# Performance work log

Measured on AMD Instinct MI355X. Metric: run time of the kernel, lower is better.

Reference implementation:

```python
import jax, jax.numpy as jnp
import numpy as np

DIM = 2048
N_HEADS = 16
Q_LORA = 1536
KV_LORA = 512
NOPE = 128
ROPE = 64
V_DIM = 128
QK_HEAD = NOPE + ROPE
SEQ = 4096
THETA = 10000.0
EPS = 1e-6
SCALE = QK_HEAD ** -0.5  # max_seq_len==4096 not >4096, so no mscale adjustment


def rms_norm(x, w):
    return x * jax.lax.rsqrt(jnp.mean(x * x, axis=-1, keepdims=True) + EPS) * w


def rope_cos_sin(seqlen):
    inv_freq = 1.0 / THETA ** (jnp.arange(0, ROPE, 2, dtype=jnp.float32) / ROPE)  # [ROPE/2]
    t = jnp.arange(seqlen, dtype=jnp.float32)
    freqs = jnp.outer(t, inv_freq)  # [S, ROPE/2]
    return jnp.cos(freqs), jnp.sin(freqs)


def apply_rope(x, cos, sin):
    # x: (b, s, h, ROPE); pairs (x0, x1) rotated as complex mult, interleaved layout
    b, s, h, d = x.shape
    xr = x.reshape(b, s, h, d // 2, 2)
    x0, x1 = xr[..., 0], xr[..., 1]
    c = cos[None, :, None, :]
    sn = sin[None, :, None, :]
    out = jnp.stack([x0 * c - x1 * sn, x0 * sn + x1 * c], axis=-1)
    return out.reshape(b, s, h, d)


def setup_inputs() -> dict:
    key = jax.random.key(0)
    ks = jax.random.split(key, 8)
    s = lambda fan_in: 1.0 / np.sqrt(fan_in)
    return {
        "x": jax.random.normal(ks[0], (1, SEQ, DIM), jnp.float32),
        "wq_a_w": jax.random.normal(ks[1], (Q_LORA, DIM), jnp.float32) * s(DIM),
        "q_norm_w": 1.0 + 0.02 * jax.random.normal(ks[2], (Q_LORA,), jnp.float32),
        "wq_b_w": jax.random.normal(ks[3], (N_HEADS * QK_HEAD, Q_LORA), jnp.float32) * s(Q_LORA),
        "wkv_a_w": jax.random.normal(ks[4], (KV_LORA + ROPE, DIM), jnp.float32) * s(DIM),
        "kv_norm_w": 1.0 + 0.02 * jax.random.normal(ks[5], (KV_LORA,), jnp.float32),
        "wkv_b_w": jax.random.normal(ks[6], (N_HEADS * (NOPE + V_DIM), KV_LORA), jnp.float32) * s(KV_LORA),
        "wo_w": jax.random.normal(ks[7], (DIM, DIM), jnp.float32) * s(DIM),
    }


def reference(x, wq_a_w, q_norm_w, wq_b_w, wkv_a_w, kv_norm_w, wkv_b_w, wo_w):
    b, seqlen, _ = x.shape
    cos, sin = rope_cos_sin(seqlen)

    # Q path: low-rank down-proj -> RMSNorm -> up-proj
    q = rms_norm(x @ wq_a_w.T, q_norm_w) @ wq_b_w.T
    q = q.reshape(b, seqlen, N_HEADS, QK_HEAD)
    q_nope, q_pe = q[..., :NOPE], q[..., NOPE:]
    q_pe = apply_rope(q_pe, cos, sin)

    # KV path: compressed latent + decoupled rope key
    kv_a = x @ wkv_a_w.T  # (b, s, KV_LORA + ROPE)
    kv_latent, k_pe_raw = kv_a[..., :KV_LORA], kv_a[..., KV_LORA:]
    kv = rms_norm(kv_latent, kv_norm_w)               # (b, t, c)
    k_pe = apply_rope(k_pe_raw[:, :, None, :], cos, sin)[:, :, 0, :]  # (b, t, r)

    # Absorption trick: fold wkv_b's K-part into q_nope, attend against latents
    wkv_b = wkv_b_w.reshape(N_HEADS, NOPE + V_DIM, KV_LORA)
    q_abs = jnp.einsum("bshd,hdc->bshc", q_nope, wkv_b[:, :NOPE])

    scores = (jnp.einsum("bshc,btc->bsht", q_abs, kv)
              + jnp.einsum("bshr,btr->bsht", q_pe, k_pe)) * SCALE

    # causal additive mask over (s_query, t_key)
    causal = jnp.tril(jnp.ones((seqlen, seqlen), dtype=bool))
    scores = jnp.where(causal[None, :, None, :], scores, jnp.float32(-1e30))
    attn = jax.nn.softmax(scores, axis=-1)

    # post-softmax: aggregate latents, then recover V via wkv_b's V-part
    ctx = jnp.einsum("bsht,btc->bshc", attn, kv)
    v = jnp.einsum("bshc,hdc->bshd", ctx, wkv_b[:, NOPE:])  # (b, s, h, V_DIM)
    out = v.reshape(b, seqlen, N_HEADS * V_DIM) @ wo_w.T
    return out
```

## Files before the change

kernel.cpp:

```cpp
#include <hip/hip_runtime.h>

typedef unsigned short u16;
typedef __attribute__((ext_vector_type(8))) short bf16x8;
typedef __attribute__((ext_vector_type(4))) float f32x4;
typedef __attribute__((ext_vector_type(4))) unsigned short u16x4;

#define MFMA16(a, b, c) __builtin_amdgcn_mfma_f32_16x16x32_bf16((a), (b), (c), 0, 0, 0)

#define SEQ 4096
#define SCALE 0.07216878364870323f
#define LOGTHETA 9.210340371976184f

__device__ __forceinline__ u16 f2bf(float f) {
  union { float f; unsigned u; } c; c.f = f;
  unsigned u = c.u;
  unsigned r = (u + 0x7fffu + ((u >> 16) & 1u)) >> 16;
  return (u16)r;
}
__device__ __forceinline__ float bf2f(u16 b) {
  union { unsigned u; float f; } c; c.u = ((unsigned)b) << 16;
  return c.f;
}

__global__ void cvt_bf16(const float* __restrict__ src, u16* __restrict__ dst, int n4) {
  int stride = gridDim.x * blockDim.x;
  for (int i = blockIdx.x * blockDim.x + threadIdx.x; i < n4; i += stride) {
    f32x4 v = ((const f32x4*)src)[i];
    u16x4 o;
    o[0] = f2bf(v[0]); o[1] = f2bf(v[1]); o[2] = f2bf(v[2]); o[3] = f2bf(v[3]);
    ((u16x4*)dst)[i] = o;
  }
}

__global__ void trans_wkvb(const u16* __restrict__ w, u16* __restrict__ wt) {
  int stride = gridDim.x * blockDim.x;
  for (int i = blockIdx.x * blockDim.x + threadIdx.x; i < 16 * 512 * 128; i += stride) {
    int h = i >> 16;
    int r = i & 65535;
    int c = r >> 7, d = r & 127;
    wt[i] = w[(h * 256 + d) * 512 + c];
  }
}

__global__ void trans_vt(const u16* __restrict__ kva, u16* __restrict__ vt2) {
  __shared__ u16 tile[64][65];
  int c0 = blockIdx.x * 64;
  int t0 = blockIdx.y * 64;
  for (int k = 0; k < 16; k++) {
    int el = threadIdx.x + k * 256;
    int r = el >> 6, c = el & 63;
    tile[r][c] = kva[(t0 + r) * 576 + c0 + c];
  }
  __syncthreads();
  for (int k = 0; k < 16; k++) {
    int el = threadIdx.x + k * 256;
    int r = el >> 6, c = el & 63;
    int t = t0 + c;
    vt2[(t >> 5) * 16384 + (c0 + r) * 32 + (t & 31)] = tile[c][r];
  }
}

__global__ void rms_q_kernel(u16* __restrict__ qa, const float* __restrict__ w) {
  int row = blockIdx.x;
  u16* p = qa + row * 1536;
  float vals[6];
  float ss = 0.f;
#pragma unroll
  for (int k = 0; k < 6; k++) {
    float v = bf2f(p[threadIdx.x + k * 256]);
    vals[k] = v;
    ss += v * v;
  }
  for (int m = 1; m < 64; m <<= 1) ss += __shfl_xor(ss, m);
  __shared__ float red[4];
  int wid = threadIdx.x >> 6;
  if ((threadIdx.x & 63) == 0) red[wid] = ss;
  __syncthreads();
  float tot = red[0] + red[1] + red[2] + red[3];
  float rr = rsqrtf(tot / 1536.f + 1e-6f);
#pragma unroll
  for (int k = 0; k < 6; k++) {
    int i = threadIdx.x + k * 256;
    p[i] = f2bf(vals[k] * rr * w[i]);
  }
}

__global__ void rms_kv_kernel(u16* __restrict__ kva, const float* __restrict__ w) {
  int t = blockIdx.x;
  u16* p = kva + t * 576;
  float v0 = bf2f(p[threadIdx.x]);
  float v1 = bf2f(p[threadIdx.x + 256]);
  float ss = v0 * v0 + v1 * v1;
  for (int m = 1; m < 64; m <<= 1) ss += __shfl_xor(ss, m);
  __shared__ float red[4];
  int wid = threadIdx.x >> 6;
  if ((threadIdx.x & 63) == 0) red[wid] = ss;
  __syncthreads();
  float tot = red[0] + red[1] + red[2] + red[3];
  float rr = rsqrtf(tot / 512.f + 1e-6f);
  p[threadIdx.x] = f2bf(v0 * rr * w[threadIdx.x]);
  p[threadIdx.x + 256] = f2bf(v1 * rr * w[threadIdx.x + 256]);
  if (threadIdx.x < 32) {
    int i = threadIdx.x;
    float x0 = bf2f(p[512 + 2 * i]);
    float x1 = bf2f(p[512 + 2 * i + 1]);
    float invf = expf(-((float)(2 * i) / 64.f) * LOGTHETA);
    float ang = (float)t * invf;
    float cs = cosf(ang), sn = sinf(ang);
    p[512 + 2 * i] = f2bf(x0 * cs - x1 * sn);
    p[512 + 2 * i + 1] = f2bf(x0 * sn + x1 * cs);
  }
}

__global__ void rope_q_kernel(const u16* __restrict__ qb, u16* __restrict__ qcat) {
  int stride = gridDim.x * blockDim.x;
  for (int idx = blockIdx.x * blockDim.x + threadIdx.x; idx < 4096 * 512; idx += stride) {
    int s = idx >> 9;
    int r = idx & 511;
    int h = r >> 5, i = r & 31;
    float x0 = bf2f(qb[s * 3072 + h * 192 + 128 + 2 * i]);
    float x1 = bf2f(qb[s * 3072 + h * 192 + 128 + 2 * i + 1]);
    float invf = expf(-((float)(2 * i) / 64.f) * LOGTHETA);
    float ang = (float)s * invf;
    float cs = cosf(ang) * SCALE, sn = sinf(ang) * SCALE;
    qcat[s * 9216 + h * 576 + 512 + 2 * i] = f2bf(x0 * cs - x1 * sn);
    qcat[s * 9216 + h * 576 + 512 + 2 * i + 1] = f2bf(x0 * sn + x1 * cs);
  }
}

template <int BN, bool OUTF32>
__launch_bounds__(256)
__global__ void gemm_tiled(const u16* __restrict__ A, int lda, int az,
                           const u16* __restrict__ W, int ldw, int wz,
                           void* __restrict__ Cp, int ldc, int cz, int K, float oscale) {
  constexpr int NCH = 8 + BN / 16;
  constexpr int NBF = BN / 32;
  __shared__ __align__(16) u16 lds[2][NCH * 512];

  int z = blockIdx.z;
  int wid = threadIdx.x >> 6, lane = threadIdx.x & 63;
  int quad = lane >> 4, l16 = lane & 15;
  int wr = wid >> 1, wc = wid & 1;
  int m0 = blockIdx.y * 128;
  int n0 = blockIdx.x * BN;

  const u16* Az = A + (size_t)z * az;
  const u16* Wz = W + (size_t)z * wz;

  f32x4 acc[4][NBF];
#pragma unroll
  for (int i = 0; i < 4; i++)
#pragma unroll
    for (int j = 0; j < NBF; j++) acc[i][j] = {0.f, 0.f, 0.f, 0.f};

#pragma unroll
  for (int jj = 0; jj < NCH / 4; jj++) {
    int c = jj * 4 + wid;
    const u16* src = (c < 8) ? (Az + (m0 + c * 16 + l16) * (size_t)lda + quad * 8)
                             : (Wz + (n0 + (c - 8) * 16 + l16) * (size_t)ldw + quad * 8);
    __builtin_amdgcn_global_load_lds(
        (const __attribute__((address_space(1))) unsigned int*)src,
        (__attribute__((address_space(3))) unsigned int*)&lds[0][c * 512], 16, 0, 0);
  }

  int buf = 0;
  for (int k0 = 0; k0 < K; k0 += 32) {
    __syncthreads();
    if (k0 + 32 < K) {
      int k1 = k0 + 32;
#pragma unroll
      for (int jj = 0; jj < NCH / 4; jj++) {
        int c = jj * 4 + wid;
        const u16* src = (c < 8) ? (Az + (m0 + c * 16 + l16) * (size_t)lda + k1 + quad * 8)
                                 : (Wz + (n0 + (c - 8) * 16 + l16) * (size_t)ldw + k1 + quad * 8);
        __builtin_amdgcn_global_load_lds(
            (const __attribute__((address_space(1))) unsigned int*)src,
            (__attribute__((address_space(3))) unsigned int*)&lds[buf ^ 1][c * 512], 16, 0, 0);
      }
    }
    const u16* base = &lds[buf][0];
    bf16x8 a[4], b[NBF];
#pragma unroll
    for (int i = 0; i < 4; i++)
      a[i] = *(const bf16x8*)(base + (wr * 4 + i) * 512 + lane * 8);
#pragma unroll
    for (int j = 0; j < NBF; j++)
      b[j] = *(const bf16x8*)(base + (8 + wc * NBF + j) * 512 + lane * 8);
#pragma unroll
    for (int i = 0; i < 4; i++)
#pragma unroll
      for (int j = 0; j < NBF; j++) acc[i][j] = MFMA16(a[i], b[j], acc[i][j]);
    buf ^= 1;
  }

#pragma unroll
  for (int i = 0; i < 4; i++) {
    int row = m0 + wr * 64 + i * 16 + quad * 4;
#pragma unroll
    for (int j = 0; j < NBF; j++) {
      int col = n0 + wc * (BN / 2) + j * 16 + l16;
#pragma unroll
      for (int r = 0; r < 4; r++) {
        size_t cbase = (size_t)z * cz + (size_t)(row + r) * ldc + col;
        if (OUTF32) ((float*)Cp)[cbase] = acc[i][j][r] * oscale;
        else        ((u16*)Cp)[cbase] = f2bf(acc[i][j][r] * oscale);
      }
    }
  }
}

__launch_bounds__(512, 2)
__global__ void attn_kernel(const u16* __restrict__ qcat, const u16* __restrict__ kcat,
                            const u16* __restrict__ vt2, u16* __restrict__ ctx) {
  __shared__ __align__(16) u16 lds[2][34816];
  __shared__ __align__(16) u16 plds[8][16][40];

  int wid = threadIdx.x >> 6, lane = threadIdx.x & 63;
  int quad = lane >> 4, l16 = lane & 15;
  int bx = blockIdx.x;
  int h = bx & 15;
  int jb = 31 - (bx >> 4);
  int qb0 = jb << 7;
  int m0 = qb0 + wid * 16;

  bf16x8 q[18];
  {
    const u16* qb = qcat + (m0 + l16) * 9216 + h * 576 + quad * 8;
#pragma unroll
    for (int kk = 0; kk < 18; kk++) q[kk] = *(const bf16x8*)(qb + kk * 32);
  }

  f32x4 zero = {0.f, 0.f, 0.f, 0.f};
  f32x4 o[32];
#pragma unroll
  for (int ct = 0; ct < 32; ct++) o[ct] = zero;
  float li[4] = {0.f, 0.f, 0.f, 0.f};

  int nt = (qb0 >> 5) + 4;

  const u16* sp[9];
  int sstr[9], soff[9];
  bool sact[9];
#pragma unroll
  for (int jj = 0; jj < 9; jj++) {
    int c = jj * 8 + wid;
    sact[jj] = (c < 68);
    soff[jj] = c * 512;
    if (c < 36) {
      int kk = c >> 1, half = c & 1;
      sp[jj] = kcat + (half * 16 + l16) * 576 + kk * 32 + quad * 8;
      sstr[jj] = 32 * 576;
    } else {
      int ct = c - 36;
      sp[jj] = vt2 + (ct * 16 + l16) * 32 + quad * 8;
      sstr[jj] = 16384;
    }
  }

#pragma unroll
  for (int jj = 0; jj < 9; jj++) {
    if (sact[jj]) {
      __builtin_amdgcn_global_load_lds(
          (const __attribute__((address_space(1))) unsigned int*)sp[jj],
          (__attribute__((address_space(3))) unsigned int*)&lds[0][soff[jj]], 16, 0, 0);
      sp[jj] += sstr[jj];
    }
  }

  for (int ti = 0; ti < nt; ti++) {
    __syncthreads();
    int buf = ti & 1;
    if (ti + 1 < nt) {
      u16* dbase = &lds[buf ^ 1][0];
#pragma unroll
      for (int jj = 0; jj < 9; jj++) {
        if (sact[jj]) {
          __builtin_amdgcn_global_load_lds(
              (const __attribute__((address_space(1))) unsigned int*)sp[jj],
              (__attribute__((address_space(3))) unsigned int*)&dbase[soff[jj]], 16, 0, 0);
          sp[jj] += sstr[jj];
        }
      }
    }

    int t0 = ti << 5;
    if (t0 <= m0 + 15) {
      const u16* kb = &lds[buf][0];
      const u16* vb = &lds[buf][18432];
      f32x4 s0 = zero, s1 = zero;
#pragma unroll
      for (int kk = 0; kk < 18; kk++) {
        bf16x8 b0 = *(const bf16x8*)(&kb[(kk * 2 + 0) * 512 + lane * 8]);
        bf16x8 b1 = *(const bf16x8*)(&kb[(kk * 2 + 1) * 512 + lane * 8]);
        s0 = MFMA16(q[kk], b0, s0);
        s1 = MFMA16(q[kk], b1, s1);
      }
      int tc0 = t0 + l16, tc1 = t0 + 16 + l16;
#pragma unroll
      for (int r = 0; r < 4; r++) {
        int mrow = m0 + quad * 4 + r;
        float e0 = (tc0 <= mrow) ? __expf(s0[r]) : 0.f;
        float e1 = (tc1 <= mrow) ? __expf(s1[r]) : 0.f;
        li[r] += e0 + e1;
        plds[wid][quad * 4 + r][l16] = f2bf(e0);
        plds[wid][quad * 4 + r][16 + l16] = f2bf(e1);
      }
      __threadfence_block();
      bf16x8 ap = *(const bf16x8*)(&plds[wid][l16][quad * 8]);
#pragma unroll
      for (int ct = 0; ct < 32; ct++) {
        bf16x8 bv = *(const bf16x8*)(&vb[ct * 512 + lane * 8]);
        o[ct] = MFMA16(ap, bv, o[ct]);
      }
    }
  }

#pragma unroll
  for (int r = 0; r < 4; r++) {
    float s = li[r];
    s += __shfl_xor(s, 1);
    s += __shfl_xor(s, 2);
    s += __shfl_xor(s, 4);
    s += __shfl_xor(s, 8);
    li[r] = s;
  }
  f32x4 inv = {1.f / li[0], 1.f / li[1], 1.f / li[2], 1.f / li[3]};
#pragma unroll
  for (int ct = 0; ct < 32; ct++) {
    f32x4 val = o[ct] * inv;
    int base = (m0 + quad * 4) * 8192 + h * 512 + ct * 16 + l16;
    ctx[base] = f2bf(val[0]);
    ctx[base + 8192] = f2bf(val[1]);
    ctx[base + 2 * 8192] = f2bf(val[2]);
    ctx[base + 3 * 8192] = f2bf(val[3]);
  }
}

extern "C" void kernel_launch(void* const* d_in, const int* in_sizes, int n_in,
                              void* d_out, int out_size, void* d_ws, size_t ws_size,
                              hipStream_t stream) {
  const float* x = (const float*)d_in[0];
  const float* wqa = (const float*)d_in[1];
  const float* qnw = (const float*)d_in[2];
  const float* wqb = (const float*)d_in[3];
  const float* wkva = (const float*)d_in[4];
  const float* kvnw = (const float*)d_in[5];
  const float* wkvb = (const float*)d_in[6];
  const float* wo = (const float*)d_in[7];

  u16* ws = (u16*)d_ws;
  u16* XB = ws;
  u16* WQAB = ws + 8388608;
  u16* WQBB = ws + 11534336;
  u16* WKVAB = ws + 16252928;
  u16* WKVBB = ws + 17432576;
  u16* WKVBT = ws + 19529728;
  u16* WOB = ws + 20578304;
  u16* QA = ws + 24772608;
  u16* KVA = ws + 31064064;
  u16* VT = ws + 33423360;
  u16* QCAT = ws + 35520512;
  u16* CTX = ws + 73269248;
  u16* QB = CTX;
  u16* VBUF = QCAT;

  dim3 blk(256);

  cvt_bf16<<<1024, blk, 0, stream>>>(x, XB, 2097152);
  cvt_bf16<<<1024, blk, 0, stream>>>(wqa, WQAB, 786432);
  cvt_bf16<<<1024, blk, 0, stream>>>(wqb, WQBB, 1179648);
  cvt_bf16<<<1024, blk, 0, stream>>>(wkva, WKVAB, 294912);
  cvt_bf16<<<1024, blk, 0, stream>>>(wkvb, WKVBB, 524288);
  cvt_bf16<<<1024, blk, 0, stream>>>(wo, WOB, 1048576);
  trans_wkvb<<<1024, blk, 0, stream>>>(WKVBB, WKVBT);

  gemm_tiled<128, false><<<dim3(12, 32, 1), blk, 0, stream>>>(XB, 2048, 0, WQAB, 2048, 0, QA, 1536, 0, 2048, 1.f);
  gemm_tiled<64, false><<<dim3(9, 32, 1), blk, 0, stream>>>(XB, 2048, 0, WKVAB, 2048, 0, KVA, 576, 0, 2048, 1.f);

  rms_q_kernel<<<4096, blk, 0, stream>>>(QA, qnw);
  rms_kv_kernel<<<4096, blk, 0, stream>>>(KVA, kvnw);
  trans_vt<<<dim3(8, 64), blk, 0, stream>>>(KVA, VT);

  gemm_tiled<128, false><<<dim3(24, 32, 1), blk, 0, stream>>>(QA, 1536, 0, WQBB, 1536, 0, QB, 3072, 0, 1536, 1.f);

  gemm_tiled<128, false><<<dim3(4, 32, 16), blk, 0, stream>>>(QB, 3072, 192, WKVBT, 128, 65536, QCAT, 9216, 576, 128, SCALE);
  rope_q_kernel<<<2048, blk, 0, stream>>>(QB, QCAT);

  attn_kernel<<<512, dim3(512), 0, stream>>>(QCAT, KVA, VT, CTX);

  gemm_tiled<128, false><<<dim3(1, 32, 16), blk, 0, stream>>>(CTX, 8192, 512, WKVBB + 65536, 512, 131072, VBUF, 2048, 128, 512, 1.f);

  gemm_tiled<128, true><<<dim3(16, 32, 1), blk, 0, stream>>>(VBUF, 2048, 0, WOB, 2048, 0, d_out, 2048, 0, 2048, 1.f);
}
```

Measured before the change: 928.2 us.

## Split PV stage by output columns across waves with shared P tile

In the attention kernel, the P·V stage now has each wave own 64 latent columns for all 128 query rows, instead of all 512 columns for its own 16 rows. Probabilities go through a block-wide shared-memory tile behind an extra barrier. Each wave therefore loads only 4 V fragments per tile and keeps them in registers, rather than reading all 32 V fragments from LDS. The QK loop uses two accumulator chains and s_setprio around the MFMA sections, and the final normalisation reads per-row inverse sums from LDS. The cost is one extra __syncthreads per key tile and coupling between waves that have different causal extents.

```diff
diff --git a/kernel.cpp b/kernel.cpp
--- a/kernel.cpp
+++ b/kernel.cpp
@@ -213,7 +213,8 @@
 __global__ void attn_kernel(const u16* __restrict__ qcat, const u16* __restrict__ kcat,
                             const u16* __restrict__ vt2, u16* __restrict__ ctx) {
   __shared__ __align__(16) u16 lds[2][34816];
-  __shared__ __align__(16) u16 plds[8][16][40];
+  __shared__ __align__(16) u16 plds[128][40];
+  __shared__ __align__(16) float linv[128];
 
   int wid = threadIdx.x >> 6, lane = threadIdx.x & 63;
   int quad = lane >> 4, l16 = lane & 15;
@@ -222,6 +223,7 @@
   int jb = 31 - (bx >> 4);
   int qb0 = jb << 7;
   int m0 = qb0 + wid * 16;
+  int cw0 = wid << 6;
 
   bf16x8 q[18];
   {
@@ -231,9 +233,11 @@
   }
 
   f32x4 zero = {0.f, 0.f, 0.f, 0.f};
-  f32x4 o[32];
-#pragma unroll
-  for (int ct = 0; ct < 32; ct++) o[ct] = zero;
+  f32x4 o[8][4];
+#pragma unroll
+  for (int rt = 0; rt < 8; rt++)
+#pragma unroll
+    for (int ct = 0; ct < 4; ct++) o[rt][ct] = zero;
   float li[4] = {0.f, 0.f, 0.f, 0.f};
 
   int nt = (qb0 >> 5) + 4;
@@ -286,15 +290,22 @@
     int t0 = ti << 5;
     if (t0 <= m0 + 15) {
       const u16* kb = &lds[buf][0];
-      const u16* vb = &lds[buf][18432];
-      f32x4 s0 = zero, s1 = zero;
-#pragma unroll
-      for (int kk = 0; kk < 18; kk++) {
-        bf16x8 b0 = *(const bf16x8*)(&kb[(kk * 2 + 0) * 512 + lane * 8]);
-        bf16x8 b1 = *(const bf16x8*)(&kb[(kk * 2 + 1) * 512 + lane * 8]);
-        s0 = MFMA16(q[kk], b0, s0);
-        s1 = MFMA16(q[kk], b1, s1);
-      }
+      f32x4 s0a = zero, s0b = zero, s1a = zero, s1b = zero;
+      __builtin_amdgcn_s_setprio(1);
+#pragma unroll
+      for (int kk = 0; kk < 18; kk += 2) {
+        bf16x8 b00 = *(const bf16x8*)(&kb[(kk * 2 + 0) * 512 + lane * 8]);
+        bf16x8 b01 = *(const bf16x8*)(&kb[(kk * 2 + 1) * 512 + lane * 8]);
+        bf16x8 b10 = *(const bf16x8*)(&kb[(kk * 2 + 2) * 512 + lane * 8]);
+        bf16x8 b11 = *(const bf16x8*)(&kb[(kk * 2 + 3) * 512 + lane * 8]);
+        s0a = MFMA16(q[kk], b00, s0a);
+        s1a = MFMA16(q[kk], b01, s1a);
+        s0b = MFMA16(q[kk + 1], b10, s0b);
+        s1b = MFMA16(q[kk + 1], b11, s1b);
+      }
+      __builtin_amdgcn_s_setprio(0);
+      f32x4 s0 = s0a + s0b;
+      f32x4 s1 = s1a + s1b;
       int tc0 = t0 + l16, tc1 = t0 + 16 + l16;
 #pragma unroll
       for (int r = 0; r < 4; r++) {
@@ -302,16 +313,31 @@
         float e0 = (tc0 <= mrow) ? __expf(s0[r]) : 0.f;
         float e1 = (tc1 <= mrow) ? __expf(s1[r]) : 0.f;
         li[r] += e0 + e1;
-        plds[wid][quad * 4 + r][l16] = f2bf(e0);
-        plds[wid][quad * 4 + r][16 + l16] = f2bf(e1);
-      }
-      __threadfence_block();
-      bf16x8 ap = *(const bf16x8*)(&plds[wid][l16][quad * 8]);
-#pragma unroll
-      for (int ct = 0; ct < 32; ct++) {
-        bf16x8 bv = *(const bf16x8*)(&vb[ct * 512 + lane * 8]);
-        o[ct] = MFMA16(ap, bv, o[ct]);
-      }
+        int rb = (wid << 4) + quad * 4 + r;
+        plds[rb][l16] = f2bf(e0);
+        plds[rb][16 + l16] = f2bf(e1);
+      }
+    }
+    __syncthreads();
+
+    {
+      const u16* vb = &lds[buf][18432];
+      bf16x8 bv0 = *(const bf16x8*)(&vb[(cw0 / 16 + 0) * 512 + lane * 8]);
+      bf16x8 bv1 = *(const bf16x8*)(&vb[(cw0 / 16 + 1) * 512 + lane * 8]);
+      bf16x8 bv2 = *(const bf16x8*)(&vb[(cw0 / 16 + 2) * 512 + lane * 8]);
+      bf16x8 bv3 = *(const bf16x8*)(&vb[(cw0 / 16 + 3) * 512 + lane * 8]);
+      __builtin_amdgcn_s_setprio(1);
+#pragma unroll
+      for (int rt = 0; rt < 8; rt++) {
+        if (t0 <= qb0 + rt * 16 + 15) {
+          bf16x8 ap = *(const bf16x8*)(&plds[rt * 16 + l16][quad * 8]);
+          o[rt][0] = MFMA16(ap, bv0, o[rt][0]);
+          o[rt][1] = MFMA16(ap, bv1, o[rt][1]);
+          o[rt][2] = MFMA16(ap, bv2, o[rt][2]);
+          o[rt][3] = MFMA16(ap, bv3, o[rt][3]);
+        }
+      }
+      __builtin_amdgcn_s_setprio(0);
     }
   }
 
@@ -324,15 +350,23 @@
     s += __shfl_xor(s, 8);
     li[r] = s;
   }
-  f32x4 inv = {1.f / li[0], 1.f / li[1], 1.f / li[2], 1.f / li[3]};
-#pragma unroll
-  for (int ct = 0; ct < 32; ct++) {
-    f32x4 val = o[ct] * inv;
-    int base = (m0 + quad * 4) * 8192 + h * 512 + ct * 16 + l16;
-    ctx[base] = f2bf(val[0]);
-    ctx[base + 8192] = f2bf(val[1]);
-    ctx[base + 2 * 8192] = f2bf(val[2]);
-    ctx[base + 3 * 8192] = f2bf(val[3]);
+  if (l16 == 0) {
+#pragma unroll
+    for (int r = 0; r < 4; r++) linv[(wid << 4) + quad * 4 + r] = 1.f / li[r];
+  }
+  __syncthreads();
+#pragma unroll
+  for (int rt = 0; rt < 8; rt++) {
+    f32x4 iv = *(const f32x4*)(&linv[rt * 16 + quad * 4]);
+#pragma unroll
+    for (int ct = 0; ct < 4; ct++) {
+      f32x4 val = o[rt][ct];
+      int base = (qb0 + rt * 16 + quad * 4) * 8192 + h * 512 + cw0 + ct * 16 + l16;
+      ctx[base] = f2bf(val[0] * iv[0]);
+      ctx[base + 8192] = f2bf(val[1] * iv[1]);
+      ctx[base + 2 * 8192] = f2bf(val[2] * iv[2]);
+      ctx[base + 3 * 8192] = f2bf(val[3] * iv[3]);
+    }
   }
 }
 
```

New measurement: 1.015 ms. 9.3% more time.

## Compute QK scores with 32x32 MFMA split across wave pairs

Applied to the files above, without the earlier changes.

The score computation moves from two 16x16x32 MFMAs per k-step in each wave to a 32x32x16 MFMA. Each pair of waves shares a 32-row query group, and each wave covers half of the 576-wide reduction dimension. The partial scores are exchanged through LDS and summed, which halves per-wave QK MFMA work and the K fragment reads. In exchange it adds an LDS exchange plus a block-wide barrier on every tile, a shared-memory path for the row sums, and extra synchronisation that could stall waves whose causal work has already ended.

```diff
diff --git a/kernel.cpp b/kernel.cpp
--- a/kernel.cpp
+++ b/kernel.cpp
@@ -3,9 +3,11 @@
 typedef unsigned short u16;
 typedef __attribute__((ext_vector_type(8))) short bf16x8;
 typedef __attribute__((ext_vector_type(4))) float f32x4;
+typedef __attribute__((ext_vector_type(16))) float f32x16;
 typedef __attribute__((ext_vector_type(4))) unsigned short u16x4;
 
 #define MFMA16(a, b, c) __builtin_amdgcn_mfma_f32_16x16x32_bf16((a), (b), (c), 0, 0, 0)
+#define MFMA32(a, b, c) __builtin_amdgcn_mfma_f32_32x32x16_bf16((a), (b), (c), 0, 0, 0)
 
 #define SEQ 4096
 #define SCALE 0.07216878364870323f
@@ -213,28 +215,32 @@
 __global__ void attn_kernel(const u16* __restrict__ qcat, const u16* __restrict__ kcat,
                             const u16* __restrict__ vt2, u16* __restrict__ ctx) {
   __shared__ __align__(16) u16 lds[2][34816];
-  __shared__ __align__(16) u16 plds[8][16][40];
+  __shared__ __align__(16) float exch[4][32][32];
+  __shared__ __align__(16) float linv[128];
 
   int wid = threadIdx.x >> 6, lane = threadIdx.x & 63;
   int quad = lane >> 4, l16 = lane & 15;
+  int l32 = lane & 31, hi = lane >> 5;
+  int pg = wid >> 1, ws = wid & 1;
   int bx = blockIdx.x;
   int h = bx & 15;
   int jb = 31 - (bx >> 4);
   int qb0 = jb << 7;
   int m0 = qb0 + wid * 16;
+  int pgm0 = qb0 + pg * 32;
 
   bf16x8 q[18];
   {
-    const u16* qb = qcat + (m0 + l16) * 9216 + h * 576 + quad * 8;
-#pragma unroll
-    for (int kk = 0; kk < 18; kk++) q[kk] = *(const bf16x8*)(qb + kk * 32);
+    const u16* qb = qcat + (size_t)(pgm0 + l32) * 9216 + h * 576 + ws * 288 + hi * 8;
+#pragma unroll
+    for (int kk = 0; kk < 18; kk++) q[kk] = *(const bf16x8*)(qb + kk * 16);
   }
 
   f32x4 zero = {0.f, 0.f, 0.f, 0.f};
   f32x4 o[32];
 #pragma unroll
   for (int ct = 0; ct < 32; ct++) o[ct] = zero;
-  float li[4] = {0.f, 0.f, 0.f, 0.f};
+  float li[8] = {0.f, 0.f, 0.f, 0.f, 0.f, 0.f, 0.f, 0.f};
 
   int nt = (qb0 >> 5) + 4;
 
@@ -247,8 +253,7 @@
     sact[jj] = (c < 68);
     soff[jj] = c * 512;
     if (c < 36) {
-      int kk = c >> 1, half = c & 1;
-      sp[jj] = kcat + (half * 16 + l16) * 576 + kk * 32 + quad * 8;
+      sp[jj] = kcat + (size_t)l32 * 576 + c * 16 + hi * 8;
       sstr[jj] = 32 * 576;
     } else {
       int ct = c - 36;
@@ -284,29 +289,66 @@
     }
 
     int t0 = ti << 5;
-    if (t0 <= m0 + 15) {
+    bool pact = (t0 <= pgm0 + 31);
+    f32x16 s;
+    if (pact) {
       const u16* kb = &lds[buf][0];
+      s = (f32x16){0.f, 0.f, 0.f, 0.f, 0.f, 0.f, 0.f, 0.f,
+                   0.f, 0.f, 0.f, 0.f, 0.f, 0.f, 0.f, 0.f};
+#pragma unroll
+      for (int kk = 0; kk < 18; kk++) {
+        bf16x8 kf = *(const bf16x8*)(&kb[(ws * 18 + kk) * 512 + lane * 8]);
+        s = MFMA32(q[kk], kf, s);
+      }
+      if (ws == 0) {
+#pragma unroll
+        for (int r8 = 0; r8 < 8; r8++) {
+          int rowl = (r8 & 3) + 8 * (r8 >> 2) + 4 * hi;
+          exch[pg][16 + rowl][l32] = s[r8 + 8];
+        }
+      } else {
+#pragma unroll
+        for (int r8 = 0; r8 < 8; r8++) {
+          int rowl = (r8 & 3) + 8 * (r8 >> 2) + 4 * hi;
+          exch[pg][rowl][l32] = s[r8];
+        }
+      }
+    }
+    asm volatile("s_waitcnt lgkmcnt(0)" ::: "memory");
+    __builtin_amdgcn_s_barrier();
+    __builtin_amdgcn_sched_barrier(0);
+
+    if (pact) {
       const u16* vb = &lds[buf][18432];
-      f32x4 s0 = zero, s1 = zero;
-#pragma unroll
-      for (int kk = 0; kk < 18; kk++) {
-        bf16x8 b0 = *(const bf16x8*)(&kb[(kk * 2 + 0) * 512 + lane * 8]);
-        bf16x8 b1 = *(const bf16x8*)(&kb[(kk * 2 + 1) * 512 + lane * 8]);
-        s0 = MFMA16(q[kk], b0, s0);
-        s1 = MFMA16(q[kk], b1, s1);
-      }
-      int tc0 = t0 + l16, tc1 = t0 + 16 + l16;
-#pragma unroll
-      for (int r = 0; r < 4; r++) {
-        int mrow = m0 + quad * 4 + r;
-        float e0 = (tc0 <= mrow) ? __expf(s0[r]) : 0.f;
-        float e1 = (tc1 <= mrow) ? __expf(s1[r]) : 0.f;
-        li[r] += e0 + e1;
-        plds[wid][quad * 4 + r][l16] = f2bf(e0);
-        plds[wid][quad * 4 + r][16 + l16] = f2bf(e1);
+      u16* Pu = (u16*)&exch[pg][ws * 16][0];
+      int tc = t0 + l32;
+      float ev[8];
+      if (ws == 0) {
+#pragma unroll
+        for (int r8 = 0; r8 < 8; r8++) {
+          int rowl = (r8 & 3) + 8 * (r8 >> 2) + 4 * hi;
+          float v = s[r8] + exch[pg][rowl][l32];
+          float e = (tc <= pgm0 + rowl) ? __expf(v) : 0.f;
+          li[r8] += e;
+          ev[r8] = e;
+        }
+      } else {
+#pragma unroll
+        for (int r8 = 0; r8 < 8; r8++) {
+          int rowl = (r8 & 3) + 8 * (r8 >> 2) + 4 * hi;
+          float v = s[r8 + 8] + exch[pg][16 + rowl][l32];
+          float e = (tc <= pgm0 + 16 + rowl) ? __expf(v) : 0.f;
+          li[r8] += e;
+          ev[r8] = e;
+        }
+      }
+#pragma unroll
+      for (int r8 = 0; r8 < 8; r8++) {
+        int rowl = (r8 & 3) + 8 * (r8 >> 2) + 4 * hi;
+        Pu[rowl * 40 + l32] = f2bf(ev[r8]);
       }
       __threadfence_block();
-      bf16x8 ap = *(const bf16x8*)(&plds[wid][l16][quad * 8]);
+      bf16x8 ap = *(const bf16x8*)(&Pu[l16 * 40 + quad * 8]);
 #pragma unroll
       for (int ct = 0; ct < 32; ct++) {
         bf16x8 bv = *(const bf16x8*)(&vb[ct * 512 + lane * 8]);
@@ -316,23 +358,32 @@
   }
 
 #pragma unroll
-  for (int r = 0; r < 4; r++) {
-    float s = li[r];
-    s += __shfl_xor(s, 1);
-    s += __shfl_xor(s, 2);
-    s += __shfl_xor(s, 4);
-    s += __shfl_xor(s, 8);
-    li[r] = s;
-  }
-  f32x4 inv = {1.f / li[0], 1.f / li[1], 1.f / li[2], 1.f / li[3]};
+  for (int r8 = 0; r8 < 8; r8++) {
+    float sum = li[r8];
+    sum += __shfl_xor(sum, 1);
+    sum += __shfl_xor(sum, 2);
+    sum += __shfl_xor(sum, 4);
+    sum += __shfl_xor(sum, 8);
+    sum += __shfl_xor(sum, 16);
+    li[r8] = sum;
+  }
+  if (l32 == 0) {
+#pragma unroll
+    for (int r8 = 0; r8 < 8; r8++) {
+      int rowl = (r8 & 3) + 8 * (r8 >> 2) + 4 * hi;
+      linv[wid * 16 + rowl] = 1.f / li[r8];
+    }
+  }
+  __syncthreads();
+  f32x4 iv = *(const f32x4*)(&linv[wid * 16 + quad * 4]);
 #pragma unroll
   for (int ct = 0; ct < 32; ct++) {
-    f32x4 val = o[ct] * inv;
+    f32x4 val = o[ct];
     int base = (m0 + quad * 4) * 8192 + h * 512 + ct * 16 + l16;
-    ctx[base] = f2bf(val[0]);
-    ctx[base + 8192] = f2bf(val[1]);
-    ctx[base + 2 * 8192] = f2bf(val[2]);
-    ctx[base + 3 * 8192] = f2bf(val[3]);
+    ctx[base] = f2bf(val[0] * iv[0]);
+    ctx[base + 8192] = f2bf(val[1] * iv[1]);
+    ctx[base + 2 * 8192] = f2bf(val[2] * iv[2]);
+    ctx[base + 3 * 8192] = f2bf(val[3] * iv[3]);
   }
 }
 
```

Result: slower. 1.214 ms (+30.8%).

## Split attention LDS into single K and V buffers with staggered prefetch

Applied to the files above, without the earlier changes.

Replaces the double-buffered combined K/V LDS tile with single K and V buffers. V for the current tile is loaded at the start of each iteration, and the next K tile is loaded after the QK MFMAs finish, behind an explicit waitcnt and barrier. This roughly halves LDS use, which may allow more blocks per CU, but it exposes V-load latency before the PV MFMAs. It also remaps block indices so heads are interleaved across query blocks for better L2 locality, and adds setprio around the MFMA loops.

```diff
diff --git a/kernel.cpp b/kernel.cpp
--- a/kernel.cpp
+++ b/kernel.cpp
@@ -212,14 +212,16 @@
 __launch_bounds__(512, 2)
 __global__ void attn_kernel(const u16* __restrict__ qcat, const u16* __restrict__ kcat,
                             const u16* __restrict__ vt2, u16* __restrict__ ctx) {
-  __shared__ __align__(16) u16 lds[2][34816];
+  __shared__ __align__(16) u16 kbuf[18432];
+  __shared__ __align__(16) u16 vbuf[16384];
   __shared__ __align__(16) u16 plds[8][16][40];
+  __shared__ __align__(16) float linv[128];
 
   int wid = threadIdx.x >> 6, lane = threadIdx.x & 63;
   int quad = lane >> 4, l16 = lane & 15;
   int bx = blockIdx.x;
-  int h = bx & 15;
-  int jb = 31 - (bx >> 4);
+  int h = (bx >> 3) & 15;
+  int jb = 31 - (((bx >> 7) << 3) | (bx & 7));
   int qb0 = jb << 7;
   int m0 = qb0 + wid * 16;
 
@@ -238,63 +240,76 @@
 
   int nt = (qb0 >> 5) + 4;
 
-  const u16* sp[9];
-  int sstr[9], soff[9];
-  bool sact[9];
-#pragma unroll
-  for (int jj = 0; jj < 9; jj++) {
+  const u16* kp[5]; int koff[5]; bool kact[5];
+#pragma unroll
+  for (int jj = 0; jj < 5; jj++) {
     int c = jj * 8 + wid;
-    sact[jj] = (c < 68);
-    soff[jj] = c * 512;
-    if (c < 36) {
-      int kk = c >> 1, half = c & 1;
-      sp[jj] = kcat + (half * 16 + l16) * 576 + kk * 32 + quad * 8;
-      sstr[jj] = 32 * 576;
-    } else {
-      int ct = c - 36;
-      sp[jj] = vt2 + (ct * 16 + l16) * 32 + quad * 8;
-      sstr[jj] = 16384;
-    }
-  }
-
-#pragma unroll
-  for (int jj = 0; jj < 9; jj++) {
-    if (sact[jj]) {
+    kact[jj] = (c < 36);
+    koff[jj] = c * 512;
+    int kk = c >> 1, half = c & 1;
+    kp[jj] = kcat + (half * 16 + l16) * 576 + kk * 32 + quad * 8;
+  }
+  const u16* vp[4]; int voff[4];
+#pragma unroll
+  for (int jj = 0; jj < 4; jj++) {
+    int c = jj * 8 + wid;
+    voff[jj] = c * 512;
+    vp[jj] = vt2 + (c * 16 + l16) * 32 + quad * 8;
+  }
+
+#pragma unroll
+  for (int jj = 0; jj < 5; jj++) {
+    if (kact[jj]) {
       __builtin_amdgcn_global_load_lds(
-          (const __attribute__((address_space(1))) unsigned int*)sp[jj],
-          (__attribute__((address_space(3))) unsigned int*)&lds[0][soff[jj]], 16, 0, 0);
-      sp[jj] += sstr[jj];
+          (const __attribute__((address_space(1))) unsigned int*)kp[jj],
+          (__attribute__((address_space(3))) unsigned int*)&kbuf[koff[jj]], 16, 0, 0);
+      kp[jj] += 32 * 576;
     }
   }
 
   for (int ti = 0; ti < nt; ti++) {
     __syncthreads();
-    int buf = ti & 1;
-    if (ti + 1 < nt) {
-      u16* dbase = &lds[buf ^ 1][0];
-#pragma unroll
-      for (int jj = 0; jj < 9; jj++) {
-        if (sact[jj]) {
-          __builtin_amdgcn_global_load_lds(
-              (const __attribute__((address_space(1))) unsigned int*)sp[jj],
-              (__attribute__((address_space(3))) unsigned int*)&dbase[soff[jj]], 16, 0, 0);
-          sp[jj] += sstr[jj];
-        }
-      }
+
+#pragma unroll
+    for (int jj = 0; jj < 4; jj++) {
+      __builtin_amdgcn_global_load_lds(
+          (const __attribute__((address_space(1))) unsigned int*)vp[jj],
+          (__attribute__((address_space(3))) unsigned int*)&vbuf[voff[jj]], 16, 0, 0);
+      vp[jj] += 16384;
     }
 
     int t0 = ti << 5;
-    if (t0 <= m0 + 15) {
-      const u16* kb = &lds[buf][0];
-      const u16* vb = &lds[buf][18432];
-      f32x4 s0 = zero, s1 = zero;
+    bool act = (t0 <= m0 + 15);
+    f32x4 s0 = zero, s1 = zero;
+    if (act) {
+      __builtin_amdgcn_s_setprio(1);
 #pragma unroll
       for (int kk = 0; kk < 18; kk++) {
-        bf16x8 b0 = *(const bf16x8*)(&kb[(kk * 2 + 0) * 512 + lane * 8]);
-        bf16x8 b1 = *(const bf16x8*)(&kb[(kk * 2 + 1) * 512 + lane * 8]);
+        bf16x8 b0 = *(const bf16x8*)(&kbuf[(kk * 2 + 0) * 512 + lane * 8]);
+        bf16x8 b1 = *(const bf16x8*)(&kbuf[(kk * 2 + 1) * 512 + lane * 8]);
         s0 = MFMA16(q[kk], b0, s0);
         s1 = MFMA16(q[kk], b1, s1);
       }
+      __builtin_amdgcn_s_setprio(0);
+    }
+
+    asm volatile("s_waitcnt vmcnt(0) lgkmcnt(0)" ::: "memory");
+    __builtin_amdgcn_s_barrier();
+    __builtin_amdgcn_sched_barrier(0);
+
+    if (ti + 1 < nt) {
+#pragma unroll
+      for (int jj = 0; jj < 5; jj++) {
+        if (kact[jj]) {
+          __builtin_amdgcn_global_load_lds(
+              (const __attribute__((address_space(1))) unsigned int*)kp[jj],
+              (__attribute__((address_space(3))) unsigned int*)&kbuf[koff[jj]], 16, 0, 0);
+          kp[jj] += 32 * 576;
+        }
+      }
+    }
+
+    if (act) {
       int tc0 = t0 + l16, tc1 = t0 + 16 + l16;
 #pragma unroll
       for (int r = 0; r < 4; r++) {
@@ -307,11 +322,13 @@
       }
       __threadfence_block();
       bf16x8 ap = *(const bf16x8*)(&plds[wid][l16][quad * 8]);
+      __builtin_amdgcn_s_setprio(1);
 #pragma unroll
       for (int ct = 0; ct < 32; ct++) {
-        bf16x8 bv = *(const bf16x8*)(&vb[ct * 512 + lane * 8]);
+        bf16x8 bv = *(const bf16x8*)(&vbuf[ct * 512 + lane * 8]);
         o[ct] = MFMA16(ap, bv, o[ct]);
       }
+      __builtin_amdgcn_s_setprio(0);
     }
   }
 
@@ -334,6 +351,7 @@
     ctx[base + 2 * 8192] = f2bf(val[2]);
     ctx[base + 3 * 8192] = f2bf(val[3]);
   }
+  (void)linv;
 }
 
 extern "C" void kernel_launch(void* const* d_in, const int* in_sizes, int n_in,
```

Result: slower. 1.095 ms (+17.9%).
